# Kernel tuning notes

Measured on AMD Instinct MI355X. Metric: run time of the kernel, lower is better.

The kernel has to match this reference:

```python
import jax, jax.numpy as jnp
import numpy as np

DIM = 384
H = 6
D = DIM // H
MLP = 4 * DIM
SCALE = D ** -0.5
LN_EPS = 1e-5


def _ln(x, w, b):
    m = jnp.mean(x, axis=-1, keepdims=True)
    v = jnp.mean((x - m) ** 2, axis=-1, keepdims=True)
    return (x - m) * jax.lax.rsqrt(v + LN_EPS) * w + b


def setup_inputs() -> dict:
    key = jax.random.key(0)
    ks = jax.random.split(key, 8)
    B, N = 8, 1024
    x = jax.random.normal(ks[0], (B, N, DIM), dtype=jnp.float32)
    # torch nn.Linear weights are [out, in]
    qkv_w = jax.random.normal(ks[1], (3 * DIM, DIM), dtype=jnp.float32) * (DIM ** -0.5)
    proj_w = jax.random.normal(ks[2], (DIM, DIM), dtype=jnp.float32) * (DIM ** -0.5)
    proj_b = jnp.zeros((DIM,), jnp.float32)
    # L2Q params, 'quadratic' init
    alpha = jnp.full((H, 1, 1), 0.125, jnp.float32)
    beta = jnp.full((H, 1, 1), 0.5, jnp.float32)
    gamma = jnp.zeros((H, 1, 1), jnp.float32)
    ln1_w = jnp.ones((DIM,), jnp.float32)
    ln1_b = jnp.zeros((DIM,), jnp.float32)
    ln2_w = jnp.ones((DIM,), jnp.float32)
    ln2_b = jnp.zeros((DIM,), jnp.float32)
    w1 = jax.random.normal(ks[3], (MLP, DIM), dtype=jnp.float32) * (DIM ** -0.5)
    b1 = jnp.zeros((MLP,), jnp.float32)
    w2 = jax.random.normal(ks[4], (DIM, MLP), dtype=jnp.float32) * (MLP ** -0.5)
    b2 = jnp.zeros((DIM,), jnp.float32)
    return {"x": x, "qkv_w": qkv_w, "proj_w": proj_w, "proj_b": proj_b,
            "alpha": alpha, "beta": beta, "gamma": gamma,
            "ln1_w": ln1_w, "ln1_b": ln1_b, "ln2_w": ln2_w, "ln2_b": ln2_b,
            "w1": w1, "b1": b1, "w2": w2, "b2": b2}


def reference(x, qkv_w, proj_w, proj_b, alpha, beta, gamma,
              ln1_w, ln1_b, ln2_w, ln2_b, w1, b1, w2, b2):
    B, N, C = x.shape
    # --- L2Q attention on LN(x) ---
    h = _ln(x, ln1_w, ln1_b)
    qkv = (h @ qkv_w.T).reshape(B, N, 3, H, D)
    q = qkv[:, :, 0].transpose(0, 2, 1, 3)  # [B,H,N,D]
    k = qkv[:, :, 1].transpose(0, 2, 1, 3)
    v = qkv[:, :, 2].transpose(0, 2, 1, 3)
    logits = jnp.einsum('bhnd,bhmd->bhnm', q, k) * SCALE
    attn = jax.nn.relu(alpha * logits ** 2 + beta * logits + gamma)
    attn = attn / (jnp.sum(attn, axis=-1, keepdims=True) + 1e-6)
    out = jnp.einsum('bhnm,bhmd->bhnd', attn, v)
    out = out.transpose(0, 2, 1, 3).reshape(B, N, C)
    x = x + out @ proj_w.T + proj_b
    # --- MLP on LN(x), exact GELU (torch default) ---
    h2 = _ln(x, ln2_w, ln2_b)
    m = jax.nn.gelu(h2 @ w1.T + b1, approximate=False)
    x = x + m @ w2.T + b2
    return x
```

## Files before the change

kernel.cpp:

```cpp
#include <hip/hip_runtime.h>
#include <hip/hip_bf16.h>
#include <math.h>

#define DIMC 384
#define NH 6
#define HD 64
#define MLPD 1536
#define BS 8
#define SEQ 1024
#define T_TOK (BS*SEQ)
#define TC ((size_t)T_TOK*DIMC)
#define QK_SCALE 0.125f

typedef __bf16 bf16;
typedef bf16 bf16x4 __attribute__((ext_vector_type(4)));
typedef bf16 bf16x8 __attribute__((ext_vector_type(8)));
typedef float floatx4 __attribute__((ext_vector_type(4)));

__device__ __forceinline__ void async_cp16(const void* gsrc, void* ldst) {
    __builtin_amdgcn_global_load_lds(
        (const __attribute__((address_space(1))) unsigned int*)gsrc,
        (__attribute__((address_space(3))) unsigned int*)ldst,
        16, 0, 0);
}

__global__ __launch_bounds__(256)
void cvt_all(const float* __restrict__ s0, const float* __restrict__ s1,
             const float* __restrict__ s2, const float* __restrict__ s3,
             bf16* __restrict__ dst) {
    int i = blockIdx.x * 256 + threadIdx.x;
    const int n0 = 110592, n1 = 36864, n2 = 147456;
    const float4* src; int j;
    if (i < n0)           { src = (const float4*)s0; j = i; }
    else if (i < n0+n1)   { src = (const float4*)s1; j = i - n0; }
    else if (i < n0+n1+n2){ src = (const float4*)s2; j = i - n0 - n1; }
    else                  { src = (const float4*)s3; j = i - n0 - n1 - n2; }
    float4 v = src[j];
    bf16x4 o; o[0] = (bf16)v.x; o[1] = (bf16)v.y; o[2] = (bf16)v.z; o[3] = (bf16)v.w;
    ((bf16x4*)dst)[i] = o;
}

__global__ __launch_bounds__(256)
void ln_kernel(const float* __restrict__ x, const float* __restrict__ w,
               const float* __restrict__ b, bf16* __restrict__ out) {
    int row = blockIdx.x * 4 + (threadIdx.x >> 6);
    int t = threadIdx.x & 63;
    const float* xr = x + (size_t)row * DIMC;
    float vals[6];
    float s = 0.f;
    #pragma unroll
    for (int i = 0; i < 6; i++) { vals[i] = xr[t + i*64]; s += vals[i]; }
    #pragma unroll
    for (int m = 32; m; m >>= 1) s += __shfl_xor(s, m);
    float mean = s * (1.0f / DIMC);
    float sq = 0.f;
    #pragma unroll
    for (int i = 0; i < 6; i++) { float d = vals[i] - mean; sq += d * d; }
    #pragma unroll
    for (int m = 32; m; m >>= 1) sq += __shfl_xor(sq, m);
    float rstd = rsqrtf(sq * (1.0f / DIMC) + 1e-5f);
    bf16* orow = out + (size_t)row * DIMC;
    #pragma unroll
    for (int i = 0; i < 6; i++) {
        int c = t + i*64;
        orow[c] = (bf16)((vals[i] - mean) * rstd * w[c] + b[c]);
    }
}

__global__ __launch_bounds__(256)
void ln2_fused(const float* __restrict__ x, const bf16* __restrict__ p0,
               const bf16* __restrict__ p1, const float* __restrict__ pb,
               const float* __restrict__ w, const float* __restrict__ b,
               float* __restrict__ x1, bf16* __restrict__ h) {
    int row = blockIdx.x * 4 + (threadIdx.x >> 6);
    int t = threadIdx.x & 63;
    size_t base = (size_t)row * DIMC;
    float vals[6];
    float s = 0.f;
    #pragma unroll
    for (int i = 0; i < 6; i++) {
        int c = t + i*64;
        float v = x[base + c] + (float)p0[base + c] + (float)p1[base + c] + pb[c];
        vals[i] = v; s += v;
    }
    #pragma unroll
    for (int m = 32; m; m >>= 1) s += __shfl_xor(s, m);
    float mean = s * (1.0f / DIMC);
    float sq = 0.f;
    #pragma unroll
    for (int i = 0; i < 6; i++) { float d = vals[i] - mean; sq += d * d; }
    #pragma unroll
    for (int m = 32; m; m >>= 1) sq += __shfl_xor(sq, m);
    float rstd = rsqrtf(sq * (1.0f / DIMC) + 1e-5f);
    #pragma unroll
    for (int i = 0; i < 6; i++) {
        int c = t + i*64;
        x1[base + c] = vals[i];
        h[base + c] = (bf16)((vals[i] - mean) * rstd * w[c] + b[c]);
    }
}

__global__ __launch_bounds__(256)
void reduce4(float* __restrict__ xo, const bf16* __restrict__ p0, const bf16* __restrict__ p1,
             const bf16* __restrict__ p2, const bf16* __restrict__ p3,
             const float* __restrict__ b2) {
    int i = blockIdx.x * 256 + threadIdx.x;
    float4 v = ((const float4*)xo)[i];
    int c = (i % 96) * 4;
    float4 bb = *(const float4*)(b2 + c);
    bf16x4 a0 = ((const bf16x4*)p0)[i], a1 = ((const bf16x4*)p1)[i];
    bf16x4 a2 = ((const bf16x4*)p2)[i], a3 = ((const bf16x4*)p3)[i];
    v.x += bb.x + (float)a0[0] + (float)a1[0] + (float)a2[0] + (float)a3[0];
    v.y += bb.y + (float)a0[1] + (float)a1[1] + (float)a2[1] + (float)a3[1];
    v.z += bb.z + (float)a0[2] + (float)a1[2] + (float)a2[2] + (float)a3[2];
    v.w += bb.w + (float)a0[3] + (float)a1[3] + (float)a2[3] + (float)a3[3];
    ((float4*)xo)[i] = v;
}

enum { EPI_NONE = 0, EPI_QKV = 1, EPI_GELU = 3 };

template<int EPI, int K, int KS, typename OutT>
__global__ __launch_bounds__(256)
void gemm_bt(const bf16* __restrict__ A, const bf16* __restrict__ W,
             const float* __restrict__ bias, OutT* out, int M, int N) {
    __shared__ __align__(16) bf16 Ash[128*32];
    __shared__ __align__(16) bf16 Bsh[128*32];
    constexpr int KB = K / KS;
    int tid = threadIdx.x;
    int lane = tid & 63, w = tid >> 6;
    int quad = lane >> 4, l16 = lane & 15;
    int rbase = blockIdx.y * 128 + (w >> 1) * 64;
    int cbase = blockIdx.x * 128 + (w & 1) * 64;
    int kbase = blockIdx.z * KB;
    int c1 = w * 64 + lane;
    int c2 = c1 + 256;
    const bf16* Ag1 = A + (size_t)(blockIdx.y*128 + (c1 >> 2)) * K + kbase + (c1 & 3) * 8;
    const bf16* Ag2 = A + (size_t)(blockIdx.y*128 + (c2 >> 2)) * K + kbase + (c2 & 3) * 8;
    const bf16* Wg1 = W + (size_t)(blockIdx.x*128 + (c1 >> 2)) * K + kbase + (c1 & 3) * 8;
    const bf16* Wg2 = W + (size_t)(blockIdx.x*128 + (c2 >> 2)) * K + kbase + (c2 & 3) * 8;
    bf16* As1 = Ash + c1 * 8;  bf16* As2 = Ash + c2 * 8;
    bf16* Bs1 = Bsh + c1 * 8;  bf16* Bs2 = Bsh + c2 * 8;

    int arow = (w >> 1) * 64;
    int brow = (w & 1) * 64;
    floatx4 acc[4][4] = {};
    #pragma unroll
    for (int kk = 0; kk < KB / 32; kk++) {
        __syncthreads();
        async_cp16(Ag1 + kk*32, As1);
        async_cp16(Ag2 + kk*32, As2);
        async_cp16(Wg1 + kk*32, Bs1);
        async_cp16(Wg2 + kk*32, Bs2);
        __syncthreads();
        bf16x8 a[4], bfr[4];
        #pragma unroll
        for (int tm = 0; tm < 4; tm++)
            a[tm] = *(const bf16x8*)&Ash[(arow + tm*16 + l16) * 32 + quad*8];
        #pragma unroll
        for (int tn = 0; tn < 4; tn++)
            bfr[tn] = *(const bf16x8*)&Bsh[(brow + tn*16 + l16) * 32 + quad*8];
        #pragma unroll
        for (int tm = 0; tm < 4; tm++)
            #pragma unroll
            for (int tn = 0; tn < 4; tn++)
                acc[tm][tn] = __builtin_amdgcn_mfma_f32_16x16x32_bf16(a[tm], bfr[tn], acc[tm][tn], 0, 0, 0);
    }

    #pragma unroll
    for (int tm = 0; tm < 4; tm++)
        #pragma unroll
        for (int tn = 0; tn < 4; tn++) {
            if constexpr (EPI == EPI_QKV) {
                int colb = cbase + tn*16 + l16;
                int which = colb / 384;
                int rowb = rbase + tm*16 + quad*4;
                int bb = rowb >> 10;
                if (which == 2) {
                    int rem = colb - 768;
                    int hh = rem >> 6, d = rem & 63;
                    int n = rowb & 1023;
                    bf16x4 pk;
                    #pragma unroll
                    for (int r = 0; r < 4; r++) pk[r] = (bf16)acc[tm][tn][r];
                    *(bf16x4*)((bf16*)out + 2*TC + (((size_t)(bb*NH + hh) * HD + d) << 10) + n) = pk;
                } else {
                    int rem = colb - which*384;
                    int hh = rem >> 6, d = rem & 63;
                    #pragma unroll
                    for (int r = 0; r < 4; r++) {
                        int n = (rowb & 1023) + r;
                        ((bf16*)out)[(size_t)which*TC + (((size_t)(bb*NH + hh) * SEQ + n) << 6) + d]
                            = (bf16)acc[tm][tn][r];
                    }
                }
            } else if constexpr (EPI == EPI_NONE) {
                OutT* ob = out + (size_t)blockIdx.z * M * N;
                #pragma unroll
                for (int r = 0; r < 4; r++) {
                    int row = rbase + tm*16 + quad*4 + r;
                    int col = cbase + tn*16 + l16;
                    ob[(size_t)row * N + col] = (OutT)acc[tm][tn][r];
                }
            } else {
                #pragma unroll
                for (int r = 0; r < 4; r++) {
                    int row = rbase + tm*16 + quad*4 + r;
                    int col = cbase + tn*16 + l16;
                    float v = acc[tm][tn][r] + bias[col];
                    v = 0.5f * v * (1.0f + erff(v * 0.70710678118f));
                    out[(size_t)row * N + col] = (OutT)v;
                }
            }
        }
}

__global__ __launch_bounds__(256)
void attn_kernel(const bf16* __restrict__ q, const bf16* __restrict__ k,
                 const bf16* __restrict__ vt, const float* __restrict__ alpha,
                 const float* __restrict__ beta, const float* __restrict__ gamma,
                 bf16* __restrict__ attn_out) {
    __shared__ __align__(16) char smem[52992];
    bf16  (*Psh)[72] = (bf16(*)[72])smem;
    float (*Ored)[68] = (float(*)[68])smem;
    float* rsred = (float*)(smem + 52224);

    int L = blockIdx.x;
    int xcd = L & 7, slot = L >> 3;
    int qt = slot & 15;
    int bh = xcd + ((slot >> 4) << 3);
    int bb = bh / NH, h = bh % NH;
    int q0 = qt * 64;
    int tid = threadIdx.x;
    int w = tid >> 6, lane = tid & 63, quad = lane >> 4, l16 = lane & 15;
    float av = alpha[h] * (QK_SCALE * QK_SCALE), bv = beta[h] * QK_SCALE, gv = gamma[h];
    const bf16* qb  = q  + (size_t)bh * SEQ * HD;
    const bf16* kb  = k  + (size_t)bh * SEQ * HD;
    const bf16* vtb = vt + (size_t)bh * HD * SEQ;

    bf16x8 qa[4][2];
    #pragma unroll
    for (int tm = 0; tm < 4; tm++)
        #pragma unroll
        for (int ks = 0; ks < 2; ks++)
            qa[tm][ks] = *(const bf16x8*)(qb + (size_t)(q0 + tm*16 + l16) * HD + ks*32 + quad*8);

    bf16x8 vone;
    #pragma unroll
    for (int j = 0; j < 8; j++) vone[j] = (bf16)1.0f;

    floatx4 o[4][4] = {};
    floatx4 rsacc[4] = {};
    int prow = w * 64;
    int rd_sw = ((l16 >> 2) & 3) << 3;

    for (int kt = w*4; kt < w*4 + 4; kt++) {
        int kb0 = kt * 64;
        bf16x8 kf[2][4];
        #pragma unroll
        for (int ks = 0; ks < 2; ks++)
            #pragma unroll
            for (int tn = 0; tn < 4; tn++)
                kf[ks][tn] = *(const bf16x8*)(kb + (size_t)(kb0 + tn*16 + l16) * HD + ks*32 + quad*8);
        #pragma unroll
        for (int tm = 0; tm < 4; tm++) {
            floatx4 s[4] = {};
            #pragma unroll
            for (int ks = 0; ks < 2; ks++)
                #pragma unroll
                for (int tn = 0; tn < 4; tn++)
                    s[tn] = __builtin_amdgcn_mfma_f32_16x16x32_bf16(qa[tm][ks], kf[ks][tn], s[tn], 0, 0, 0);
            #pragma unroll
            for (int tn = 0; tn < 4; tn++)
                #pragma unroll
                for (int r = 0; r < 4; r++) {
                    float xx = s[tn][r];
                    float p = fmaxf((av*xx + bv)*xx + gv, 0.f);
                    int row = tm*16 + quad*4 + r;
                    int col = (tn*16 + l16) ^ (quad << 3);
                    Psh[prow + row][col] = (bf16)p;
                }
        }
        #pragma unroll
        for (int ks = 0; ks < 2; ks++) {
            bf16x8 vf[4], pf[4];
            #pragma unroll
            for (int tn = 0; tn < 4; tn++)
                vf[tn] = *(const bf16x8*)(vtb + (size_t)(tn*16 + l16) * SEQ + kb0 + ks*32 + quad*8);
            #pragma unroll
            for (int tm = 0; tm < 4; tm++)
                pf[tm] = *(const bf16x8*)&Psh[prow + tm*16 + l16][(ks*32 + quad*8) ^ rd_sw];
            #pragma unroll
            for (int tm = 0; tm < 4; tm++)
                rsacc[tm] = __builtin_amdgcn_mfma_f32_16x16x32_bf16(pf[tm], vone, rsacc[tm], 0, 0, 0);
            #pragma unroll
            for (int tm = 0; tm < 4; tm++)
                #pragma unroll
                for (int tn = 0; tn < 4; tn++)
                    o[tm][tn] = __builtin_amdgcn_mfma_f32_16x16x32_bf16(pf[tm], vf[tn], o[tm][tn], 0, 0, 0);
        }
    }

    __syncthreads();
    if (w) {
        #pragma unroll
        for (int tm = 0; tm < 4; tm++) {
            #pragma unroll
            for (int tn = 0; tn < 4; tn++)
                #pragma unroll
                for (int r = 0; r < 4; r++)
                    Ored[(w-1)*64 + tm*16 + quad*4 + r][tn*16 + l16] = o[tm][tn][r];
            if (l16 == 0)
                #pragma unroll
                for (int r = 0; r < 4; r++)
                    rsred[(w-1)*64 + tm*16 + quad*4 + r] = rsacc[tm][r];
        }
    }
    __syncthreads();
    if (w == 0) {
        #pragma unroll
        for (int j = 0; j < 3; j++)
            #pragma unroll
            for (int tm = 0; tm < 4; tm++) {
                #pragma unroll
                for (int tn = 0; tn < 4; tn++)
                    #pragma unroll
                    for (int r = 0; r < 4; r++)
                        o[tm][tn][r] += Ored[j*64 + tm*16 + quad*4 + r][tn*16 + l16];
                #pragma unroll
                for (int r = 0; r < 4; r++)
                    rsacc[tm][r] += rsred[j*64 + tm*16 + quad*4 + r];
            }
        #pragma unroll
        for (int tm = 0; tm < 4; tm++)
            #pragma unroll
            for (int tn = 0; tn < 4; tn++)
                #pragma unroll
                for (int r = 0; r < 4; r++) {
                    int n = q0 + tm*16 + quad*4 + r;
                    attn_out[((size_t)(bb*SEQ + n)) * DIMC + h*HD + tn*16 + l16] =
                        (bf16)(o[tm][tn][r] / (rsacc[tm][r] + 1e-6f));
                }
    }
}

extern "C" void kernel_launch(void* const* d_in, const int* in_sizes, int n_in,
                              void* d_out, int out_size, void* d_ws, size_t ws_size,
                              hipStream_t stream) {
    const float* x      = (const float*)d_in[0];
    const float* qkv_w  = (const float*)d_in[1];
    const float* proj_w = (const float*)d_in[2];
    const float* proj_b = (const float*)d_in[3];
    const float* alpha  = (const float*)d_in[4];
    const float* beta   = (const float*)d_in[5];
    const float* gamma  = (const float*)d_in[6];
    const float* ln1_w  = (const float*)d_in[7];
    const float* ln1_b  = (const float*)d_in[8];
    const float* ln2_w  = (const float*)d_in[9];
    const float* ln2_b  = (const float*)d_in[10];
    const float* w1     = (const float*)d_in[11];
    const float* b1     = (const float*)d_in[12];
    const float* w2     = (const float*)d_in[13];
    const float* b2     = (const float*)d_in[14];
    float* out = (float*)d_out;

    char* base = (char*)d_ws;
    bf16* wq_bf = (bf16*)base;
    bf16* wp_bf = wq_bf + 442368;
    bf16* w1_bf = wq_bf + 589824;
    bf16* w2_bf = wq_bf + 1179648;
    bf16* h      = (bf16*)(base + 3538944);
    bf16* qkv    = (bf16*)(base + 9830400);
    bf16* attn_o = (bf16*)(base + 28704768);
    bf16* m      = qkv;
    bf16* Pp     = (bf16*)(base + 34996224);
    bf16* Pm     = (bf16*)(base + 34996224);

    cvt_all<<<1728, 256, 0, stream>>>(qkv_w, proj_w, w1, w2, wq_bf);
    ln_kernel<<<T_TOK/4, 256, 0, stream>>>(x, ln1_w, ln1_b, h);
    gemm_bt<EPI_QKV, 384, 1, bf16><<<dim3(9, 64, 1), 256, 0, stream>>>(
        h, wq_bf, nullptr, qkv, T_TOK, 1152);
    attn_kernel<<<768, 256, 0, stream>>>(
        qkv, qkv + TC, qkv + 2*TC, alpha, beta, gamma, attn_o);
    gemm_bt<EPI_NONE, 384, 2, bf16><<<dim3(3, 64, 2), 256, 0, stream>>>(
        attn_o, wp_bf, nullptr, Pp, T_TOK, DIMC);
    ln2_fused<<<T_TOK/4, 256, 0, stream>>>(x, Pp, Pp + TC, proj_b, ln2_w, ln2_b, out, h);
    gemm_bt<EPI_GELU, 384, 1, bf16><<<dim3(12, 64, 1), 256, 0, stream>>>(
        h, w1_bf, b1, m, T_TOK, MLPD);
    gemm_bt<EPI_NONE, 1536, 4, bf16><<<dim3(3, 64, 4), 256, 0, stream>>>(
        m, w2_bf, nullptr, Pm, T_TOK, DIMC);
    reduce4<<<TC/4/256, 256, 0, stream>>>(out, Pm, Pm + TC, Pm + 2*TC, Pm + 3*TC, b2);
}
```

Before: 243.3 us.

## Split attention work by query rows per wave instead of key tiles

Each of the four waves now owns 16 query rows and loops over all 16 key tiles, replacing the split-K scheme where waves shared 64 query rows and reduced partial outputs through shared memory. This removes the cross-wave reduction, the two block barriers and the large LDS buffer. It also computes S transposed (K times Q) so P can be stored as packed 4-wide writes, and the row sum is taken with shuffles rather than a ones-vector MFMA. In exchange each wave reloads every K and V tile, raising global/L2 traffic fourfold per block, and there is less reuse of K/V fragments across query rows.

```diff
diff --git a/kernel.cpp b/kernel.cpp
--- a/kernel.cpp
+++ b/kernel.cpp
@@ -219,128 +219,87 @@
                  const bf16* __restrict__ vt, const float* __restrict__ alpha,
                  const float* __restrict__ beta, const float* __restrict__ gamma,
                  bf16* __restrict__ attn_out) {
-    __shared__ __align__(16) char smem[52992];
-    bf16  (*Psh)[72] = (bf16(*)[72])smem;
-    float (*Ored)[68] = (float(*)[68])smem;
-    float* rsred = (float*)(smem + 52224);
-
+    __shared__ __align__(16) bf16 Psh[4][16][72];
     int L = blockIdx.x;
     int xcd = L & 7, slot = L >> 3;
     int qt = slot & 15;
     int bh = xcd + ((slot >> 4) << 3);
     int bb = bh / NH, h = bh % NH;
-    int q0 = qt * 64;
     int tid = threadIdx.x;
     int w = tid >> 6, lane = tid & 63, quad = lane >> 4, l16 = lane & 15;
+    int q0w = qt * 64 + w * 16;
     float av = alpha[h] * (QK_SCALE * QK_SCALE), bv = beta[h] * QK_SCALE, gv = gamma[h];
     const bf16* qb  = q  + (size_t)bh * SEQ * HD;
     const bf16* kb  = k  + (size_t)bh * SEQ * HD;
     const bf16* vtb = vt + (size_t)bh * HD * SEQ;
 
-    bf16x8 qa[4][2];
-    #pragma unroll
-    for (int tm = 0; tm < 4; tm++)
-        #pragma unroll
-        for (int ks = 0; ks < 2; ks++)
-            qa[tm][ks] = *(const bf16x8*)(qb + (size_t)(q0 + tm*16 + l16) * HD + ks*32 + quad*8);
-
-    bf16x8 vone;
-    #pragma unroll
-    for (int j = 0; j < 8; j++) vone[j] = (bf16)1.0f;
-
-    floatx4 o[4][4] = {};
-    floatx4 rsacc[4] = {};
-    int prow = w * 64;
-    int rd_sw = ((l16 >> 2) & 3) << 3;
-
-    for (int kt = w*4; kt < w*4 + 4; kt++) {
+    bf16x8 qa[2];
+    #pragma unroll
+    for (int ks = 0; ks < 2; ks++)
+        qa[ks] = *(const bf16x8*)(qb + (size_t)(q0w + l16) * HD + ks*32 + quad*8);
+
+    floatx4 o[4] = {};
+    float rs = 0.f;
+
+    #pragma unroll 2
+    for (int kt = 0; kt < 16; kt++) {
         int kb0 = kt * 64;
         bf16x8 kf[2][4];
         #pragma unroll
         for (int ks = 0; ks < 2; ks++)
             #pragma unroll
+            for (int t = 0; t < 4; t++)
+                kf[ks][t] = *(const bf16x8*)(kb + (size_t)(kb0 + t*16 + l16) * HD + ks*32 + quad*8);
+        floatx4 s[4] = {};
+        #pragma unroll
+        for (int ks = 0; ks < 2; ks++)
+            #pragma unroll
+            for (int t = 0; t < 4; t++)
+                s[t] = __builtin_amdgcn_mfma_f32_16x16x32_bf16(kf[ks][t], qa[ks], s[t], 0, 0, 0);
+        float part = 0.f;
+        #pragma unroll
+        for (int t = 0; t < 4; t++) {
+            bf16x4 pk;
+            #pragma unroll
+            for (int r = 0; r < 4; r++) {
+                float xx = s[t][r];
+                float p = fmaxf((av*xx + bv)*xx + gv, 0.f);
+                part += p;
+                pk[r] = (bf16)p;
+            }
+            *(bf16x4*)&Psh[w][l16][t*16 + quad*4] = pk;
+        }
+        part += __shfl_xor(part, 16);
+        part += __shfl_xor(part, 32);
+        rs += part;
+        bf16x8 pf[2];
+        #pragma unroll
+        for (int ks = 0; ks < 2; ks++)
+            pf[ks] = *(const bf16x8*)&Psh[w][l16][ks*32 + quad*8];
+        bf16x8 vf[2][4];
+        #pragma unroll
+        for (int ks = 0; ks < 2; ks++)
+            #pragma unroll
             for (int tn = 0; tn < 4; tn++)
-                kf[ks][tn] = *(const bf16x8*)(kb + (size_t)(kb0 + tn*16 + l16) * HD + ks*32 + quad*8);
-        #pragma unroll
-        for (int tm = 0; tm < 4; tm++) {
-            floatx4 s[4] = {};
-            #pragma unroll
-            for (int ks = 0; ks < 2; ks++)
-                #pragma unroll
-                for (int tn = 0; tn < 4; tn++)
-                    s[tn] = __builtin_amdgcn_mfma_f32_16x16x32_bf16(qa[tm][ks], kf[ks][tn], s[tn], 0, 0, 0);
+                vf[ks][tn] = *(const bf16x8*)(vtb + (size_t)(tn*16 + l16) * SEQ + kb0 + ks*32 + quad*8);
+        #pragma unroll
+        for (int ks = 0; ks < 2; ks++)
             #pragma unroll
             for (int tn = 0; tn < 4; tn++)
-                #pragma unroll
-                for (int r = 0; r < 4; r++) {
-                    float xx = s[tn][r];
-                    float p = fmaxf((av*xx + bv)*xx + gv, 0.f);
-                    int row = tm*16 + quad*4 + r;
-                    int col = (tn*16 + l16) ^ (quad << 3);
-                    Psh[prow + row][col] = (bf16)p;
-                }
+                o[tn] = __builtin_amdgcn_mfma_f32_16x16x32_bf16(pf[ks], vf[ks][tn], o[tn], 0, 0, 0);
+    }
+
+    float rsq[4];
+    #pragma unroll
+    for (int r = 0; r < 4; r++) rsq[r] = __shfl(rs, quad*4 + r);
+    #pragma unroll
+    for (int tn = 0; tn < 4; tn++)
+        #pragma unroll
+        for (int r = 0; r < 4; r++) {
+            int n = q0w + quad*4 + r;
+            attn_out[((size_t)(bb*SEQ + n)) * DIMC + h*HD + tn*16 + l16] =
+                (bf16)(o[tn][r] / (rsq[r] + 1e-6f));
         }
-        #pragma unroll
-        for (int ks = 0; ks < 2; ks++) {
-            bf16x8 vf[4], pf[4];
-            #pragma unroll
-            for (int tn = 0; tn < 4; tn++)
-                vf[tn] = *(const bf16x8*)(vtb + (size_t)(tn*16 + l16) * SEQ + kb0 + ks*32 + quad*8);
-            #pragma unroll
-            for (int tm = 0; tm < 4; tm++)
-                pf[tm] = *(const bf16x8*)&Psh[prow + tm*16 + l16][(ks*32 + quad*8) ^ rd_sw];
-            #pragma unroll
-            for (int tm = 0; tm < 4; tm++)
-                rsacc[tm] = __builtin_amdgcn_mfma_f32_16x16x32_bf16(pf[tm], vone, rsacc[tm], 0, 0, 0);
-            #pragma unroll
-            for (int tm = 0; tm < 4; tm++)
-                #pragma unroll
-                for (int tn = 0; tn < 4; tn++)
-                    o[tm][tn] = __builtin_amdgcn_mfma_f32_16x16x32_bf16(pf[tm], vf[tn], o[tm][tn], 0, 0, 0);
-        }
-    }
-
-    __syncthreads();
-    if (w) {
-        #pragma unroll
-        for (int tm = 0; tm < 4; tm++) {
-            #pragma unroll
-            for (int tn = 0; tn < 4; tn++)
-                #pragma unroll
-                for (int r = 0; r < 4; r++)
-                    Ored[(w-1)*64 + tm*16 + quad*4 + r][tn*16 + l16] = o[tm][tn][r];
-            if (l16 == 0)
-                #pragma unroll
-                for (int r = 0; r < 4; r++)
-                    rsred[(w-1)*64 + tm*16 + quad*4 + r] = rsacc[tm][r];
-        }
-    }
-    __syncthreads();
-    if (w == 0) {
-        #pragma unroll
-        for (int j = 0; j < 3; j++)
-            #pragma unroll
-            for (int tm = 0; tm < 4; tm++) {
-                #pragma unroll
-                for (int tn = 0; tn < 4; tn++)
-                    #pragma unroll
-                    for (int r = 0; r < 4; r++)
-                        o[tm][tn][r] += Ored[j*64 + tm*16 + quad*4 + r][tn*16 + l16];
-                #pragma unroll
-                for (int r = 0; r < 4; r++)
-                    rsacc[tm][r] += rsred[j*64 + tm*16 + quad*4 + r];
-            }
-        #pragma unroll
-        for (int tm = 0; tm < 4; tm++)
-            #pragma unroll
-            for (int tn = 0; tn < 4; tn++)
-                #pragma unroll
-                for (int r = 0; r < 4; r++) {
-                    int n = q0 + tm*16 + quad*4 + r;
-                    attn_out[((size_t)(bb*SEQ + n)) * DIMC + h*HD + tn*16 + l16] =
-                        (bf16)(o[tm][tn][r] / (rsacc[tm][r] + 1e-6f));
-                }
-    }
 }
 
 extern "C" void kernel_launch(void* const* d_in, const int* in_sizes, int n_in,
```

Result: slower. 274.3 us (+12.7%).
